# Performance work log

Measured on AMD Instinct MI355X. Metric: run time of the kernel, lower is better.

The kernel has to match this reference:

```python
import jax, jax.numpy as jnp
import numpy as np

B, N, C = 4, 8192, 512
H = 4
D = C // H  # 128
HID = 4 * C  # mlp hidden, mlp_ratio=4.0
SCALE = D ** -0.5
EPS = 1e-5


def layernorm(x, w, b):
    mu = jnp.mean(x, axis=-1, keepdims=True)
    var = jnp.var(x, axis=-1, keepdims=True)
    return (x - mu) * jax.lax.rsqrt(var + EPS) * w + b


def setup_inputs() -> dict:
    key = jax.random.key(0)
    ks = jax.random.split(key, 8)
    s = lambda fan_in: 1.0 / np.sqrt(fan_in)
    return {
        "x": jax.random.normal(ks[0], (B, N, C), jnp.float32),
        "norm1_w": jnp.ones((C,), jnp.float32),
        "norm1_b": jnp.zeros((C,), jnp.float32),
        "qkv_w": jax.random.normal(ks[1], (C, 3 * C), jnp.float32) * s(C),
        "qkv_b": jnp.zeros((3 * C,), jnp.float32),
        "lnk_w": jnp.ones((D,), jnp.float32),
        "lnk_b": jnp.zeros((D,), jnp.float32),
        "lnv_w": jnp.ones((D,), jnp.float32),
        "lnv_b": jnp.zeros((D,), jnp.float32),
        "proj_w": jax.random.normal(ks[2], (C, C), jnp.float32) * s(C),
        "proj_b": jnp.zeros((C,), jnp.float32),
        "norm2_w": jnp.ones((C,), jnp.float32),
        "norm2_b": jnp.zeros((C,), jnp.float32),
        "mlp_w1": jax.random.normal(ks[3], (C, HID), jnp.float32) * s(C),
        "mlp_b1": jnp.zeros((HID,), jnp.float32),
        "mlp_w2": jax.random.normal(ks[4], (HID, C), jnp.float32) * s(HID),
        "mlp_b2": jnp.zeros((C,), jnp.float32),
    }


def reference(x, norm1_w, norm1_b, qkv_w, qkv_b, lnk_w, lnk_b, lnv_w, lnv_b,
              proj_w, proj_b, norm2_w, norm2_b, mlp_w1, mlp_b1, mlp_w2, mlp_b2):
    shortcut = x
    xn = layernorm(x, norm1_w, norm1_b)
    qkv = xn @ qkv_w + qkv_b                       # [B,N,3C]
    qkv = qkv.reshape(B, N, 3, H, D).transpose(2, 0, 3, 1, 4)  # [3,B,H,N,D]
    q, k, v = qkv[0], qkv[1], qkv[2]
    k = layernorm(k, lnk_w, lnk_b)
    v = layernorm(v, lnv_w, lnv_b)
    context = jnp.einsum('bhnd,bhne->bhde', k, v)   # [B,H,D,D] small context
    attn = jnp.einsum('bhnd,bhde->bhne', q, context) * SCALE  # [B,H,N,D]
    attn = attn.transpose(0, 2, 1, 3).reshape(B, N, C)
    x1 = shortcut + (attn @ proj_w + proj_b)
    h = layernorm(x1, norm2_w, norm2_b)
    mlp = jax.nn.gelu(h @ mlp_w1 + mlp_b1, approximate=False) @ mlp_w2 + mlp_b2
    return x1 + mlp
```

## Files before the change

### kernel.cpp

```cpp
#include <hip/hip_runtime.h>
#include <stdint.h>


#define B_    4
#define N_    8192
#define C_    512
#define H_    4
#define D_    128
#define HID_  2048
#define M_    (B_*N_)
#define EPS_  1e-5f
#define SCALE_ 0.08838834764831845f

typedef unsigned short u16;
typedef __attribute__((ext_vector_type(8))) __bf16 bfrag_t;
typedef __attribute__((ext_vector_type(4))) float  f4_t;

__device__ __forceinline__ float bf2f(u16 a) {
    unsigned int u = ((unsigned int)a) << 16; float f;
    __builtin_memcpy(&f, &u, 4); return f;
}
__device__ __forceinline__ u16 f2bf(float f) {
    unsigned int u; __builtin_memcpy(&u, &f, 4);
    u += 0x7FFFu + ((u >> 16) & 1u);
    return (u16)(u >> 16);
}
__device__ __forceinline__ u16 f2bf_fast(float f) {
    unsigned int u; __builtin_memcpy(&u, &f, 4);
    return (u16)((u + 0x8000u) >> 16);
}

__device__ __forceinline__ float fast_gelu(float x) {
    const float kA = 2.3022084f;
    const float kB = 0.1029435f;
    float x2 = x * x;
    float e1 = __builtin_amdgcn_exp2f(x * (kB * x2 + kA));
    return x - x * __builtin_amdgcn_rcpf(e1 + 1.0f);
}

__device__ __forceinline__ void gld16(u16* lds, const u16* g) {
    void* gp = const_cast<u16*>(g);
    __builtin_amdgcn_global_load_lds((__attribute__((address_space(1))) void*)gp,
                                     (__attribute__((address_space(3))) void*)lds,
                                     16, 0, 0);
}

__global__ void wtrans(const float* __restrict__ in, u16* __restrict__ out,
                       int K, int Ncols) {
    long idx = (long)blockIdx.x * 256 + threadIdx.x;
    long total = (long)K * Ncols;
    if (idx >= total) return;
    int k = (int)(idx % K), n = (int)(idx / K);
    out[idx] = f2bf(in[(long)k * Ncols + n]);
}

__global__ __launch_bounds__(256)
void ln_rows(const float* __restrict__ in, const float* __restrict__ w,
             const float* __restrict__ b, u16* __restrict__ out) {
    long row = blockIdx.x;
    int t = threadIdx.x;
    const float* p = in + row * 512;
    float v0 = p[t], v1 = p[t + 256];
    float s = v0 + v1, q = v0 * v0 + v1 * v1;
    #pragma unroll
    for (int o = 32; o >= 1; o >>= 1) { s += __shfl_xor(s, o, 64); q += __shfl_xor(q, o, 64); }
    __shared__ float sh[8];
    int wv = t >> 6, l = t & 63;
    if (l == 0) { sh[wv] = s; sh[4 + wv] = q; }
    __syncthreads();
    s = sh[0] + sh[1] + sh[2] + sh[3];
    q = sh[4] + sh[5] + sh[6] + sh[7];
    float mu = s * (1.f / 512.f);
    float var = q * (1.f / 512.f) - mu * mu;
    float rs = rsqrtf(var + EPS_);
    out[row * 512 + t]       = f2bf((v0 - mu) * rs * w[t] + b[t]);
    out[row * 512 + t + 256] = f2bf((v1 - mu) * rs * w[t + 256] + b[t + 256]);
}

__global__ __launch_bounds__(256)
void lnkv(const u16* __restrict__ qkv,
          const float* __restrict__ kw, const float* __restrict__ kb,
          const float* __restrict__ vw, const float* __restrict__ vb,
          u16* __restrict__ kT, u16* __restrict__ vT) {
    int bh = blockIdx.x;
    int b = bh >> 2, h = bh & 3;
    int n0 = blockIdx.y * 64;
    int wv = threadIdx.x >> 6, l = threadIdx.x & 63;
    __shared__ u16 lk[128 * 68], lv[128 * 68];

    for (int r = wv; r < 64; r += 4) {
        long base = ((long)b * N_ + n0 + r) * 1536 + h * 128;
        {
            float x0 = bf2f(qkv[base + 512 + l]), x1 = bf2f(qkv[base + 512 + 64 + l]);
            float s = x0 + x1, q = x0 * x0 + x1 * x1;
            #pragma unroll
            for (int o = 32; o >= 1; o >>= 1) { s += __shfl_xor(s, o, 64); q += __shfl_xor(q, o, 64); }
            float mu = s * (1.f / 128.f), var = q * (1.f / 128.f) - mu * mu;
            float rs = rsqrtf(var + EPS_);
            lk[l * 68 + r]        = f2bf((x0 - mu) * rs * kw[l] + kb[l]);
            lk[(l + 64) * 68 + r] = f2bf((x1 - mu) * rs * kw[l + 64] + kb[l + 64]);
        }
        {
            float x0 = bf2f(qkv[base + 1024 + l]), x1 = bf2f(qkv[base + 1024 + 64 + l]);
            float s = x0 + x1, q = x0 * x0 + x1 * x1;
            #pragma unroll
            for (int o = 32; o >= 1; o >>= 1) { s += __shfl_xor(s, o, 64); q += __shfl_xor(q, o, 64); }
            float mu = s * (1.f / 128.f), var = q * (1.f / 128.f) - mu * mu;
            float rs = rsqrtf(var + EPS_);
            lv[l * 68 + r]        = f2bf((x0 - mu) * rs * vw[l] + vb[l]);
            lv[(l + 64) * 68 + r] = f2bf((x1 - mu) * rs * vw[l + 64] + vb[l + 64]);
        }
    }
    __syncthreads();
    long obase = (long)bh * D_ * N_;
    #pragma unroll 4
    for (int i = 0; i < 32; i++) {
        int idx = i * 256 + threadIdx.x;
        int d = idx >> 6, nn = idx & 63;
        kT[obase + (long)d * N_ + n0 + nn] = lk[d * 68 + nn];
        vT[obase + (long)d * N_ + n0 + nn] = lv[d * 68 + nn];
    }
}

__global__ void ctxfin(const float* __restrict__ ctx, u16* __restrict__ ctxT) {
    int idx = blockIdx.x * 256 + threadIdx.x;
    if (idx >= 16 * 16384) return;
    int z = idx >> 14, r = idx & 16383;
    int e = r >> 7, d = r & 127;
    ctxT[idx] = f2bf(ctx[(z << 14) + (d << 7) + e] * SCALE_);
}

template<int MODE, int KTOT, int ZDIV>
__global__ __launch_bounds__(256)
void gemm_bt(const u16* __restrict__ A, int lda, int64_t aZ1, int64_t aZ2,
             const u16* __restrict__ Bt, int ldb, int64_t bZ1, int64_t bZ2,
             void* __restrict__ outv, int ldo, int64_t oZ1, int64_t oZ2,
             const float* __restrict__ bias, const float* __restrict__ resid, int ldr) {
    __shared__ __align__(16) u16 sA[128 * 32];
    __shared__ __align__(16) u16 sB[128 * 32];
    const int z = blockIdx.z;
    const int z1 = z / ZDIV, z2 = z % ZDIV;
    A  += z1 * aZ1 + z2 * aZ2;
    Bt += z1 * bZ1 + z2 * bZ2;
    const int64_t ooff = z1 * oZ1 + z2 * oZ2;
    const int m0 = blockIdx.x * 128, n0 = blockIdx.y * 128;
    const int tid = threadIdx.x, wave = tid >> 6, lane = tid & 63;
    const int wr = wave >> 1, wc = wave & 1;

    f4_t acc[4][4];
    #pragma unroll
    for (int i = 0; i < 4; i++)
        #pragma unroll
        for (int j = 0; j < 4; j++) acc[i][j] = (f4_t){0.f, 0.f, 0.f, 0.f};

    const int c0 = wave * 64 + lane, c1 = 256 + wave * 64 + lane;
    const int r0 = c0 >> 2, e0 = (c0 & 3) * 8;
    const int r1 = c1 >> 2, e1 = (c1 & 3) * 8;
    const u16* a0 = A + (int64_t)(m0 + r0) * lda + e0;
    const u16* a1 = A + (int64_t)(m0 + r1) * lda + e1;
    const u16* b0 = Bt + (int64_t)(n0 + r0) * ldb + e0;
    const u16* b1 = Bt + (int64_t)(n0 + r1) * ldb + e1;
    u16* lA0 = &sA[wave * 512];        u16* lA1 = &sA[2048 + wave * 512];
    u16* lB0 = &sB[wave * 512];        u16* lB1 = &sB[2048 + wave * 512];

    const int qd = lane >> 4, md = lane & 15;
    int aoff[4], boff[4];
    #pragma unroll
    for (int i = 0; i < 4; i++) {
        aoff[i] = (wr * 64 + i * 16 + md) * 32 + qd * 8;
        boff[i] = (wc * 64 + i * 16 + md) * 32 + qd * 8;
    }

    #pragma unroll 4
    for (int kt = 0; kt < KTOT; kt += 32) {
        __syncthreads();
        gld16(lA0, a0 + kt);  gld16(lA1, a1 + kt);
        gld16(lB0, b0 + kt);  gld16(lB1, b1 + kt);
        __syncthreads();
        bfrag_t af[4], bf[4];
        #pragma unroll
        for (int i = 0; i < 4; i++) af[i] = *(const bfrag_t*)&sA[aoff[i]];
        #pragma unroll
        for (int i = 0; i < 4; i++) bf[i] = *(const bfrag_t*)&sB[boff[i]];
        #pragma unroll
        for (int mi = 0; mi < 4; mi++)
            #pragma unroll
            for (int ni = 0; ni < 4; ni++)
                acc[mi][ni] = __builtin_amdgcn_mfma_f32_16x16x32_bf16(
                    af[mi], bf[ni], acc[mi][ni], 0, 0, 0);
    }

    #pragma unroll
    for (int mi = 0; mi < 4; mi++) {
        #pragma unroll
        for (int r = 0; r < 4; r++) {
            int m = m0 + wr * 64 + mi * 16 + qd * 4 + r;
            int64_t rowo = ooff + (int64_t)m * ldo;
            #pragma unroll
            for (int ni = 0; ni < 4; ni++) {
                int n = n0 + wc * 64 + ni * 16 + md;
                float v = acc[mi][ni][r];
                if (MODE == 0)
                    ((u16*)outv)[rowo + n] = f2bf_fast(v);
                else
                    atomicAdd(&((float*)outv)[rowo + n], v);
            }
        }
    }
}

#define LD_(p)      (*(const bfrag_t*)(p))
#define FENCE_      asm volatile("" ::: "memory")
#define BAR_        do { FENCE_; __builtin_amdgcn_s_barrier(); FENCE_; } while (0)
#define WAITVM0_    asm volatile("s_waitcnt vmcnt(0)" ::: "memory")
#define MFMA_(va, vb, c) c = __builtin_amdgcn_mfma_f32_16x16x32_bf16(va, vb, c, 0, 0, 0)
#define MM16_(I0) do { __builtin_amdgcn_s_setprio(1); \
  MFMA_(a0,b0,acc[(I0)+0][0]); MFMA_(a0,b1,acc[(I0)+0][1]); MFMA_(a0,b2,acc[(I0)+0][2]); MFMA_(a0,b3,acc[(I0)+0][3]); \
  MFMA_(a1,b0,acc[(I0)+1][0]); MFMA_(a1,b1,acc[(I0)+1][1]); MFMA_(a1,b2,acc[(I0)+1][2]); MFMA_(a1,b3,acc[(I0)+1][3]); \
  MFMA_(a2,b0,acc[(I0)+2][0]); MFMA_(a2,b1,acc[(I0)+2][1]); MFMA_(a2,b2,acc[(I0)+2][2]); MFMA_(a2,b3,acc[(I0)+2][3]); \
  MFMA_(a3,b0,acc[(I0)+3][0]); MFMA_(a3,b1,acc[(I0)+3][1]); MFMA_(a3,b2,acc[(I0)+3][2]); MFMA_(a3,b3,acc[(I0)+3][3]); \
  __builtin_amdgcn_s_setprio(0); } while (0)
#define STG_(r) do { \
  gld16(lds + nb * 32768 + (r) * 4096 + wid * 512,         aT + (r) * lda64); \
  gld16(lds + nb * 32768 + 16384 + (r) * 4096 + wid * 512, bT + (r) * ldb64); } while (0)

template<int MODE, int KTOT>
__global__ __launch_bounds__(512, 2)
void gemm256(const u16* __restrict__ A, int lda,
             const u16* __restrict__ Bt, int ldb,
             void* __restrict__ outv, int ldo,
             const float* __restrict__ bias, const float* __restrict__ resid, int ldr) {
    __shared__ __align__(16) u16 lds[65536];
    const int m0 = blockIdx.x * 256, n0 = blockIdx.y * 256;
    const int tid = threadIdx.x, wid = tid >> 6, lane = tid & 63;
    const int wr = wid >> 2, wc = wid & 3;
    const int md = lane & 15, qd = lane >> 4;

    f4_t acc[8][4];
    #pragma unroll
    for (int i = 0; i < 8; ++i)
        #pragma unroll
        for (int j = 0; j < 4; ++j) acc[i][j] = (f4_t){0.f, 0.f, 0.f, 0.f};

    const int srow = tid >> 3;
    const int scol = ((tid & 7) ^ (srow & 7)) * 8;
    const u16* aS = A  + (int64_t)(m0 + srow) * lda + scol;
    const u16* bS = Bt + (int64_t)(n0 + srow) * ldb + scol;
    const int64_t lda64 = (int64_t)lda * 64, ldb64 = (int64_t)ldb * 64;

    const int aRow = (wr * 128 + md) * 128;
    const int bRow = (wc * 64 + md) * 128;
    const int x0 = (qd ^ (md & 7)) * 16;
    const int x1 = ((4 + qd) ^ (md & 7)) * 16;
    const char* ldsc = (const char*)lds;

    constexpr int NT = KTOT / 64;

    {
        const int nb = 0;
        const u16* aT = aS; const u16* bT = bS;
        STG_(0); STG_(1); STG_(2); STG_(3);
        WAITVM0_; BAR_;
    }

    #pragma unroll 2
    for (int t = 0; t < NT; ++t) {
        const int cur = t & 1, nb = cur ^ 1;
        const char* cA = ldsc + cur * 65536 + aRow;
        const char* cB = ldsc + cur * 65536 + 32768 + bRow;
        const u16* aT = aS + (int64_t)(t + 1) * 64;
        const u16* bT = bS + (int64_t)(t + 1) * 64;
        const bool st = (t + 1 < NT);
        bfrag_t a0, a1, a2, a3, b0, b1, b2, b3;

        a0 = LD_(cA + x0);        a1 = LD_(cA + 2048 + x0);
        a2 = LD_(cA + 4096 + x0); a3 = LD_(cA + 6144 + x0);
        b0 = LD_(cB + x0);        b1 = LD_(cB + 2048 + x0);
        b2 = LD_(cB + 4096 + x0); b3 = LD_(cB + 6144 + x0);
        if (st) { STG_(0); STG_(1); }
        BAR_;
        MM16_(0);

        a0 = LD_(cA + 8192 + x0);  a1 = LD_(cA + 10240 + x0);
        a2 = LD_(cA + 12288 + x0); a3 = LD_(cA + 14336 + x0);
        if (st) { STG_(2); STG_(3); }
        BAR_;
        MM16_(4);

        a0 = LD_(cA + x1);        a1 = LD_(cA + 2048 + x1);
        a2 = LD_(cA + 4096 + x1); a3 = LD_(cA + 6144 + x1);
        b0 = LD_(cB + x1);        b1 = LD_(cB + 2048 + x1);
        b2 = LD_(cB + 4096 + x1); b3 = LD_(cB + 6144 + x1);
        BAR_;
        MM16_(0);

        a0 = LD_(cA + 8192 + x1);  a1 = LD_(cA + 10240 + x1);
        a2 = LD_(cA + 12288 + x1); a3 = LD_(cA + 14336 + x1);
        BAR_;
        MM16_(4);
        if (st) WAITVM0_;
        BAR_;
    }

    #pragma unroll
    for (int i = 0; i < 8; ++i) {
        #pragma unroll
        for (int rr = 0; rr < 4; ++rr) {
            const int m = m0 + wr * 128 + i * 16 + qd * 4 + rr;
            const int64_t rowo = (int64_t)m * ldo;
            #pragma unroll
            for (int j = 0; j < 4; ++j) {
                const int n = n0 + wc * 64 + j * 16 + md;
                float v = acc[i][j][rr];
                if (MODE == 1 || MODE == 2 || MODE == 3) v += bias[n];
                if (MODE == 2) v = fast_gelu(v);
                if (MODE == 3) v += resid[(int64_t)m * ldr + n];
                if (MODE == 3)
                    ((float*)outv)[rowo + n] = v;
                else
                    ((u16*)outv)[rowo + n] = f2bf_fast(v);
            }
        }
    }
}

#undef LD_
#undef FENCE_
#undef BAR_
#undef WAITVM0_
#undef MFMA_
#undef MM16_
#undef STG_

extern "C" void kernel_launch(void* const* d_in, const int* in_sizes, int n_in,
                              void* d_out, int out_size, void* d_ws, size_t ws_size,
                              hipStream_t stream) {
    const float* x      = (const float*)d_in[0];
    const float* n1w    = (const float*)d_in[1];
    const float* n1b    = (const float*)d_in[2];
    const float* qkv_w  = (const float*)d_in[3];
    const float* qkv_b  = (const float*)d_in[4];
    const float* lnk_w  = (const float*)d_in[5];
    const float* lnk_b  = (const float*)d_in[6];
    const float* lnv_w  = (const float*)d_in[7];
    const float* lnv_b  = (const float*)d_in[8];
    const float* proj_w = (const float*)d_in[9];
    const float* proj_b = (const float*)d_in[10];
    const float* n2w    = (const float*)d_in[11];
    const float* n2b    = (const float*)d_in[12];
    const float* w1     = (const float*)d_in[13];
    const float* b1     = (const float*)d_in[14];
    const float* w2     = (const float*)d_in[15];
    const float* b2     = (const float*)d_in[16];
    float* out = (float*)d_out;

    char* ws = (char*)d_ws;
    u16*  qkvWT = (u16*)(ws + 0);
    u16*  projT = (u16*)(ws + 1572864);
    u16*  w1T   = (u16*)(ws + 2097152);
    u16*  w2T   = (u16*)(ws + 4194304);
    float* ctx  = (float*)(ws + 6291456);
    u16*  ctxT  = (u16*)(ws + 7340032);
    u16*  bufA  = (u16*)(ws + 7864320);
    u16*  qkv   = (u16*)(ws + 41418752);
    u16*  hid   = (u16*)(ws + 41418752);
    u16*  kT    = (u16*)(ws + 142082048);
    u16*  vT    = (u16*)(ws + 175636480);

    dim3 blk(256);
    dim3 blk5(512);

    wtrans<<<dim3(512 * 1536 / 256), blk, 0, stream>>>(qkv_w, qkvWT, 512, 1536);
    wtrans<<<dim3(512 * 512 / 256),  blk, 0, stream>>>(proj_w, projT, 512, 512);
    wtrans<<<dim3(512 * 2048 / 256), blk, 0, stream>>>(w1, w1T, 512, 2048);
    wtrans<<<dim3(2048 * 512 / 256), blk, 0, stream>>>(w2, w2T, 2048, 512);

    ln_rows<<<dim3(M_), blk, 0, stream>>>(x, n1w, n1b, bufA);

    gemm256<1, 512><<<dim3(M_ / 256, 1536 / 256), blk5, 0, stream>>>(
        bufA, 512, qkvWT, 512, (void*)qkv, 1536, qkv_b, nullptr, 0);

    lnkv<<<dim3(B_ * H_, N_ / 64), blk, 0, stream>>>(qkv, lnk_w, lnk_b, lnv_w, lnv_b, kT, vT);

    hipMemsetAsync(ctx, 0, 16 * 128 * 128 * 4, stream);
    gemm_bt<4, 512, 16><<<dim3(1, 1, B_ * H_ * 16), blk, 0, stream>>>(
        kT, N_, (int64_t)D_ * N_, 512,  vT, N_, (int64_t)D_ * N_, 512,
        (void*)ctx, 128, 16384, 0,  nullptr, nullptr, 0);
    ctxfin<<<dim3(16 * 16384 / 256), blk, 0, stream>>>(ctx, ctxT);

    gemm_bt<0, 128, 4><<<dim3(N_ / 128, 1, B_ * H_), blk, 0, stream>>>(
        qkv, 1536, (int64_t)N_ * 1536, 128,  ctxT, 128, 4 * 16384, 16384,
        (void*)bufA, 512, (int64_t)N_ * 512, 128,  nullptr, nullptr, 0);

    gemm256<3, 512><<<dim3(M_ / 256, 512 / 256), blk5, 0, stream>>>(
        bufA, 512, projT, 512, (void*)out, 512, proj_b, x, 512);

    ln_rows<<<dim3(M_), blk, 0, stream>>>(out, n2w, n2b, bufA);

    gemm256<2, 512><<<dim3(M_ / 256, HID_ / 256), blk5, 0, stream>>>(
        bufA, 512, w1T, 512, (void*)hid, HID_, b1, nullptr, 0);

    gemm256<3, 2048><<<dim3(M_ / 256, 512 / 256), blk5, 0, stream>>>(
        hid, HID_, w2T, HID_, (void*)out, 512, b2, out, 512);
}
```

Measured before the change: 594.0 us.

## Split GEMM K-tile staging into half-K chunks with partial vmcnt waits and block swizzle

Reorganizes the 256x256 GEMM LDS layout into two 32-wide K halves so that staging of the next tile is issued per half and waited on with vmcnt(4). The first half can then be consumed while the second half is still in flight, instead of waiting on all loads at the end of each iteration. It also remaps block indices in groups of 8 along M to improve L2 reuse of the weight tiles. The change adds more barriers and depends on the load counts matching vmcnt(4) exactly, so it risks a race or a stall if the counts are wrong.

Result: faster. 562.5 us (-5.3%).

```diff
diff --git a/kernel.cpp b/kernel.cpp
--- a/kernel.cpp
+++ b/kernel.cpp
@@ -212,7 +212,8 @@
 #define LD_(p)      (*(const bfrag_t*)(p))
 #define FENCE_      asm volatile("" ::: "memory")
 #define BAR_        do { FENCE_; __builtin_amdgcn_s_barrier(); FENCE_; } while (0)
-#define WAITVM0_    asm volatile("s_waitcnt vmcnt(0)" ::: "memory")
+#define WVM4_       asm volatile("s_waitcnt vmcnt(4)" ::: "memory")
+#define WVM0_       asm volatile("s_waitcnt vmcnt(0)" ::: "memory")
 #define MFMA_(va, vb, c) c = __builtin_amdgcn_mfma_f32_16x16x32_bf16(va, vb, c, 0, 0, 0)
 #define MM16_(I0) do { __builtin_amdgcn_s_setprio(1); \
   MFMA_(a0,b0,acc[(I0)+0][0]); MFMA_(a0,b1,acc[(I0)+0][1]); MFMA_(a0,b2,acc[(I0)+0][2]); MFMA_(a0,b3,acc[(I0)+0][3]); \
@@ -220,9 +221,14 @@
   MFMA_(a2,b0,acc[(I0)+2][0]); MFMA_(a2,b1,acc[(I0)+2][1]); MFMA_(a2,b2,acc[(I0)+2][2]); MFMA_(a2,b3,acc[(I0)+2][3]); \
   MFMA_(a3,b0,acc[(I0)+3][0]); MFMA_(a3,b1,acc[(I0)+3][1]); MFMA_(a3,b2,acc[(I0)+3][2]); MFMA_(a3,b3,acc[(I0)+3][3]); \
   __builtin_amdgcn_s_setprio(0); } while (0)
-#define STG_(r) do { \
-  gld16(lds + nb * 32768 + (r) * 4096 + wid * 512,         aT + (r) * lda64); \
-  gld16(lds + nb * 32768 + 16384 + (r) * 4096 + wid * 512, bT + (r) * ldb64); } while (0)
+#define STGA_(nb, kk, tt) do { \
+  u16* d_ = lds + (nb) * 32768 + (kk) * 8192 + wid * 512; \
+  const u16* s_ = aS + (int64_t)(tt) * 64 + (kk) * 32; \
+  gld16(d_, s_); gld16(d_ + 4096, s_ + a128); } while (0)
+#define STGB_(nb, kk, tt) do { \
+  u16* d_ = lds + (nb) * 32768 + 16384 + (kk) * 8192 + wid * 512; \
+  const u16* s_ = bS + (int64_t)(tt) * 64 + (kk) * 32; \
+  gld16(d_, s_); gld16(d_ + 4096, s_ + b128); } while (0)
 
 template<int MODE, int KTOT>
 __global__ __launch_bounds__(512, 2)
@@ -231,7 +237,15 @@
              void* __restrict__ outv, int ldo,
              const float* __restrict__ bias, const float* __restrict__ resid, int ldr) {
     __shared__ __align__(16) u16 lds[65536];
-    const int m0 = blockIdx.x * 256, n0 = blockIdx.y * 256;
+    const int gx = gridDim.x, gy = gridDim.y;
+    const int lid = blockIdx.x + blockIdx.y * gx;
+    int bx, by;
+    if ((gx & 7) == 0) {
+        const int j = lid >> 3;
+        bx = (gx >> 3) * (lid & 7) + j / gy;
+        by = j % gy;
+    } else { bx = blockIdx.x; by = blockIdx.y; }
+    const int m0 = bx * 256, n0 = by * 256;
     const int tid = threadIdx.x, wid = tid >> 6, lane = tid & 63;
     const int wr = wid >> 2, wc = wid & 3;
     const int md = lane & 15, qd = lane >> 4;
@@ -242,25 +256,22 @@
         #pragma unroll
         for (int j = 0; j < 4; ++j) acc[i][j] = (f4_t){0.f, 0.f, 0.f, 0.f};
 
-    const int srow = tid >> 3;
-    const int scol = ((tid & 7) ^ (srow & 7)) * 8;
+    const int srow = tid >> 2;
+    const int scol = ((tid & 3) ^ ((tid >> 3) & 3)) * 8;
     const u16* aS = A  + (int64_t)(m0 + srow) * lda + scol;
     const u16* bS = Bt + (int64_t)(n0 + srow) * ldb + scol;
-    const int64_t lda64 = (int64_t)lda * 64, ldb64 = (int64_t)ldb * 64;
-
-    const int aRow = (wr * 128 + md) * 128;
-    const int bRow = (wc * 64 + md) * 128;
-    const int x0 = (qd ^ (md & 7)) * 16;
-    const int x1 = ((4 + qd) ^ (md & 7)) * 16;
+    const int64_t a128 = (int64_t)lda * 128, b128 = (int64_t)ldb * 128;
+
+    const int xq = (qd ^ ((md >> 1) & 3)) * 16;
+    const int aRow = (wr * 128 + md) * 64;
+    const int bRow = (wc * 64 + md) * 64;
     const char* ldsc = (const char*)lds;
 
     constexpr int NT = KTOT / 64;
 
     {
-        const int nb = 0;
-        const u16* aT = aS; const u16* bT = bS;
-        STG_(0); STG_(1); STG_(2); STG_(3);
-        WAITVM0_; BAR_;
+        STGA_(0, 0, 0); STGB_(0, 0, 0); STGA_(0, 1, 0); STGB_(0, 1, 0);
+        WVM4_; BAR_;
     }
 
     #pragma unroll 2
@@ -268,37 +279,41 @@
         const int cur = t & 1, nb = cur ^ 1;
         const char* cA = ldsc + cur * 65536 + aRow;
         const char* cB = ldsc + cur * 65536 + 32768 + bRow;
-        const u16* aT = aS + (int64_t)(t + 1) * 64;
-        const u16* bT = bS + (int64_t)(t + 1) * 64;
         const bool st = (t + 1 < NT);
         bfrag_t a0, a1, a2, a3, b0, b1, b2, b3;
 
-        a0 = LD_(cA + x0);        a1 = LD_(cA + 2048 + x0);
-        a2 = LD_(cA + 4096 + x0); a3 = LD_(cA + 6144 + x0);
-        b0 = LD_(cB + x0);        b1 = LD_(cB + 2048 + x0);
-        b2 = LD_(cB + 4096 + x0); b3 = LD_(cB + 6144 + x0);
-        if (st) { STG_(0); STG_(1); }
+        a0 = LD_(cA + xq);        a1 = LD_(cA + 1024 + xq);
+        a2 = LD_(cA + 2048 + xq); a3 = LD_(cA + 3072 + xq);
+        b0 = LD_(cB + xq);        b1 = LD_(cB + 1024 + xq);
+        b2 = LD_(cB + 2048 + xq); b3 = LD_(cB + 3072 + xq);
+        if (st) STGA_(nb, 0, t + 1);
         BAR_;
         MM16_(0);
 
-        a0 = LD_(cA + 8192 + x0);  a1 = LD_(cA + 10240 + x0);
-        a2 = LD_(cA + 12288 + x0); a3 = LD_(cA + 14336 + x0);
-        if (st) { STG_(2); STG_(3); }
+        a0 = LD_(cA + 4096 + xq); a1 = LD_(cA + 5120 + xq);
+        a2 = LD_(cA + 6144 + xq); a3 = LD_(cA + 7168 + xq);
+        if (st) STGB_(nb, 0, t + 1);
         BAR_;
         MM16_(4);
 
-        a0 = LD_(cA + x1);        a1 = LD_(cA + 2048 + x1);
-        a2 = LD_(cA + 4096 + x1); a3 = LD_(cA + 6144 + x1);
-        b0 = LD_(cB + x1);        b1 = LD_(cB + 2048 + x1);
-        b2 = LD_(cB + 4096 + x1); b3 = LD_(cB + 6144 + x1);
+        if (st) { WVM4_; } else { WVM0_; }
+        BAR_;
+
+        a0 = LD_(cA + 16384 + xq);        a1 = LD_(cA + 17408 + xq);
+        a2 = LD_(cA + 18432 + xq);        a3 = LD_(cA + 19456 + xq);
+        b0 = LD_(cB + 16384 + xq);        b1 = LD_(cB + 17408 + xq);
+        b2 = LD_(cB + 18432 + xq);        b3 = LD_(cB + 19456 + xq);
+        if (st) STGA_(nb, 1, t + 1);
         BAR_;
         MM16_(0);
 
-        a0 = LD_(cA + 8192 + x1);  a1 = LD_(cA + 10240 + x1);
-        a2 = LD_(cA + 12288 + x1); a3 = LD_(cA + 14336 + x1);
+        a0 = LD_(cA + 20480 + xq); a1 = LD_(cA + 21504 + xq);
+        a2 = LD_(cA + 22528 + xq); a3 = LD_(cA + 23552 + xq);
+        if (st) STGB_(nb, 1, t + 1);
         BAR_;
         MM16_(4);
-        if (st) WAITVM0_;
+
+        if (st) { WVM4_; } else { WVM0_; }
         BAR_;
     }
 
@@ -327,10 +342,12 @@
 #undef LD_
 #undef FENCE_
 #undef BAR_
-#undef WAITVM0_
+#undef WVM4_
+#undef WVM0_
 #undef MFMA_
 #undef MM16_
-#undef STG_
+#undef STGA_
+#undef STGB_
 
 extern "C" void kernel_launch(void* const* d_in, const int* in_sizes, int n_in,
                               void* d_out, int out_size, void* d_ws, size_t ws_size,
```
